# Kernel tuning notes

Measured on AMD Instinct MI355X. Metric: run time of the kernel, lower is better.

The kernel has to match this reference:

```python
import jax, jax.numpy as jnp
import numpy as np

N = 50000      # nodes
E = 800000     # edges per view (before self loops)
F_IN = 256     # node feature dim
H = 4          # attention heads
C = 128        # hidden dim (per-head out_channels; concat=False -> mean over heads)
V = 3          # views
NEG_SLOPE = 0.2


def gat_view(x, edge_index, W, a_src, a_dst, b):
    """PyG-style GATConv(heads=H, concat=False) + ELU. Adds self loops."""
    n = x.shape[0]
    loops = jnp.arange(n, dtype=edge_index.dtype)
    src = jnp.concatenate([edge_index[0], loops])  # [E+N]
    dst = jnp.concatenate([edge_index[1], loops])
    h = (x @ W).reshape(n, H, C)                    # [N,H,C]
    s_src = jnp.sum(h * a_src, axis=-1)             # [N,H]
    s_dst = jnp.sum(h * a_dst, axis=-1)             # [N,H]
    e = jax.nn.leaky_relu(s_src[src] + s_dst[dst], NEG_SLOPE)  # [E+N,H]
    # segment softmax over incoming edges of each destination node
    m = jax.ops.segment_max(e, dst, num_segments=n)
    m = jnp.where(jnp.isfinite(m), m, 0.0)
    ex = jnp.exp(e - m[dst])
    denom = jax.ops.segment_sum(ex, dst, num_segments=n)
    alpha = ex / jnp.maximum(denom[dst], 1e-16)     # [E+N,H]
    out = jax.ops.segment_sum(h[src] * alpha[:, :, None], dst, num_segments=n)  # [N,H,C]
    return jax.nn.elu(out.mean(axis=1) + b)         # [N,C]


def setup_inputs() -> dict:
    key = jax.random.key(0)
    ks = jax.random.split(key, 12)
    d = {
        "x": jax.random.normal(ks[0], (N, F_IN), dtype=jnp.float32),
        "edge_index0": jax.random.randint(ks[1], (2, E), 0, N, dtype=jnp.int32),
        "edge_index1": jax.random.randint(ks[2], (2, E), 0, N, dtype=jnp.int32),
        "edge_index2": jax.random.randint(ks[3], (2, E), 0, N, dtype=jnp.int32),
        "W": jax.random.normal(ks[4], (V, F_IN, H * C), dtype=jnp.float32) * 0.05,
        "a_src": jax.random.normal(ks[5], (V, H, C), dtype=jnp.float32) * 0.05,
        "a_dst": jax.random.normal(ks[6], (V, H, C), dtype=jnp.float32) * 0.05,
        "b": jnp.zeros((V, C), dtype=jnp.float32),
        "fus_w": jax.random.normal(ks[7], (C, 1), dtype=jnp.float32) * 0.05,
        "fus_b": jnp.zeros((1,), dtype=jnp.float32),
        "cls_w1": jax.random.normal(ks[8], (C, C // 2), dtype=jnp.float32) * 0.05,
        "cls_b1": jnp.zeros((C // 2,), dtype=jnp.float32),
        "cls_w2": jax.random.normal(ks[9], (C // 2, 2), dtype=jnp.float32) * 0.05,
        "cls_b2": jnp.zeros((2,), dtype=jnp.float32),
    }
    return d


def reference(x, edge_index0, edge_index1, edge_index2, W, a_src, a_dst, b,
              fus_w, fus_b, cls_w1, cls_b1, cls_w2, cls_b2):
    eis = [edge_index0, edge_index1, edge_index2]
    views = [gat_view(x, eis[v], W[v], a_src[v], a_dst[v], b[v]) for v in range(V)]
    stacked = jnp.stack(views, axis=1)                     # [N,V,C]
    scores = jnp.squeeze(stacked @ fus_w, -1) + fus_b      # [N,V]
    weights = jax.nn.softmax(scores, axis=1)               # view attention
    fused = jnp.sum(stacked * weights[..., None], axis=1)  # [N,C]
    hcls = jax.nn.relu(fused @ cls_w1 + cls_b1)            # dropout = identity (eval)
    logits = hcls @ cls_w2 + cls_b2                        # [N,2]
    return logits, weights
```

## Files before the change

### kernel.cpp

```cpp
#include <hip/hip_runtime.h>
#include <math.h>

#define NN 50000
#define EE 800000
#define FIN 256
#define HH 4
#define CC 128
#define HC 512
#define VV 3

#define NB 196
#define SPB 256
#define CAP 4608
#define EPB 8192

typedef __attribute__((ext_vector_type(8))) short short8;
typedef __attribute__((ext_vector_type(4))) float f32x4;
typedef __attribute__((ext_vector_type(2))) float f32x2;

__device__ __forceinline__ float lrelu(float x){ return x > 0.f ? x : 0.2f*x; }

__device__ __forceinline__ unsigned short f2bf(float f){
  unsigned u = __float_as_uint(f);
  u += 0x7fffu + ((u >> 16) & 1);
  return (unsigned short)(u >> 16);
}
__device__ __forceinline__ float bf2f(short b){
  return __uint_as_float(((unsigned)b & 0xffffu) << 16);
}

__device__ __forceinline__ float wave_sum64(float v){
#pragma unroll
  for (int off = 32; off; off >>= 1) v += __shfl_xor(v, off);
  return v;
}

__device__ __forceinline__ void async16(void* lds, const void* g){
  __builtin_amdgcn_global_load_lds(
      (const __attribute__((address_space(1))) unsigned*)g,
      (__attribute__((address_space(3))) unsigned*)lds, 16, 0, 0);
}

__global__ __launch_bounds__(256) void cast_x(const float* __restrict__ x,
                                              unsigned short* __restrict__ xb){
  int t = blockIdx.x * 256 + threadIdx.x;
  float4 v = *(const float4*)&x[(size_t)t * 4];
  ushort4 o;
  o.x = f2bf(v.x); o.y = f2bf(v.y); o.z = f2bf(v.z); o.w = f2bf(v.w);
  *(ushort4*)&xb[(size_t)t * 4] = o;
}

__global__ __launch_bounds__(256) void prep_w_all(const float* __restrict__ W,
                                                  unsigned short* __restrict__ wp){
  int t = blockIdx.x * 256 + threadIdx.x;
  int v = t >> 17;
  int tl = t & 131071;
  int k = tl >> 9, n = tl & 511;
  wp[(size_t)v * (FIN * HC) + (size_t)(k >> 5) * (HC * 32) + n * 32 + (k & 31)] = f2bf(W[t]);
}

__global__ __launch_bounds__(256) void gemm_mfma_scores(
    const unsigned short* __restrict__ xb, const unsigned short* __restrict__ wp_all,
    unsigned char* __restrict__ hb_all,
    const float* __restrict__ a_src, const float* __restrict__ a_dst,
    float* __restrict__ ssrc_all, float* __restrict__ sdst_all){
  __shared__ short As[128 * 32];
  __shared__ short Bs[128 * 32];
  __shared__ float sred[2][128][2];
  int tid = threadIdx.x;
  int wave = tid >> 6, lane = tid & 63;
  int l16 = lane & 15, q = lane >> 4;
  int wr = wave >> 1, wc = wave & 1;
  int head = blockIdx.y, v = blockIdx.z;
  int rowBase = blockIdx.x * 128, colBase = head * 128;

  const unsigned short* wp = wp_all + (size_t)v * FIN * HC;
  unsigned char* hb = hb_all + (size_t)v * NN * HC;
  const float* a_src_v = a_src + v * HH * CC;
  const float* a_dst_v = a_dst + v * HH * CC;
  float* ssrc = ssrc_all + (size_t)v * NN * HH;
  float* sdst = sdst_all + (size_t)v * NN * HH;

  int off0 = wave * 2048 + lane * 16;
  int off1 = off0 + 1024;
  int arow0 = off0 >> 6, akb0 = (off0 & 63) >> 1;
  int arow1 = off1 >> 6, akb1 = (off1 & 63) >> 1;
  size_t ga0 = (size_t)min(rowBase + arow0, NN - 1) * FIN + akb0;
  size_t ga1 = (size_t)min(rowBase + arow1, NN - 1) * FIN + akb1;
  const unsigned short* wpc = wp + (size_t)colBase * 32;

  f32x4 acc[4][4] = {};
  for (int kt = 0; kt < 8; kt++){
    async16((char*)As + wave * 2048,        xb + ga0 + kt * 32);
    async16((char*)As + wave * 2048 + 1024, xb + ga1 + kt * 32);
    async16((char*)Bs + wave * 2048,        wpc + (size_t)kt * (HC * 32) + (off0 >> 1));
    async16((char*)Bs + wave * 2048 + 1024, wpc + (size_t)kt * (HC * 32) + (off1 >> 1));
    __syncthreads();
    short8 af[4], bf[4];
#pragma unroll
    for (int i = 0; i < 4; i++)
      af[i] = *(const short8*)&As[(wr * 64 + i * 16 + l16) * 32 + q * 8];
#pragma unroll
    for (int j = 0; j < 4; j++)
      bf[j] = *(const short8*)&Bs[(wc * 64 + j * 16 + l16) * 32 + q * 8];
#pragma unroll
    for (int i = 0; i < 4; i++)
#pragma unroll
      for (int j = 0; j < 4; j++)
        acc[i][j] = __builtin_amdgcn_mfma_f32_16x16x32_bf16(af[i], bf[j], acc[i][j], 0, 0, 0);
    __syncthreads();
  }
#pragma unroll
  for (int i = 0; i < 4; i++){
#pragma unroll
    for (int r = 0; r < 4; r++){
      int row = rowBase + wr * 64 + i * 16 + q * 4 + r;
      if (row < NN){
        int p01 = __builtin_amdgcn_cvt_pk_fp8_f32(acc[i][0][r], acc[i][1][r], 0, false);
        int p23 = __builtin_amdgcn_cvt_pk_fp8_f32(acc[i][2][r], acc[i][3][r], 0, false);
        size_t rb = (size_t)row * HC + colBase + wc * 64 + l16;
        hb[rb +  0] = (unsigned char)(p01 & 0xff);
        hb[rb + 16] = (unsigned char)((p01 >> 8) & 0xff);
        hb[rb + 32] = (unsigned char)(p23 & 0xff);
        hb[rb + 48] = (unsigned char)((p23 >> 8) & 0xff);
      }
    }
  }
  float asv[4], adv[4];
#pragma unroll
  for (int j = 0; j < 4; j++){
    int c = wc * 64 + j * 16 + l16;
    asv[j] = a_src_v[head * CC + c];
    adv[j] = a_dst_v[head * CC + c];
  }
  float ps[4][4], pd[4][4];
#pragma unroll
  for (int i = 0; i < 4; i++)
#pragma unroll
    for (int r = 0; r < 4; r++){
      float s = 0.f, d = 0.f;
#pragma unroll
      for (int j = 0; j < 4; j++){
        s = fmaf(acc[i][j][r], asv[j], s);
        d = fmaf(acc[i][j][r], adv[j], d);
      }
      ps[i][r] = s; pd[i][r] = d;
    }
#pragma unroll
  for (int off = 1; off < 16; off <<= 1)
#pragma unroll
    for (int i = 0; i < 4; i++)
#pragma unroll
      for (int r = 0; r < 4; r++){
        ps[i][r] += __shfl_xor(ps[i][r], off);
        pd[i][r] += __shfl_xor(pd[i][r], off);
      }
  if (l16 == 0){
#pragma unroll
    for (int i = 0; i < 4; i++)
#pragma unroll
      for (int r = 0; r < 4; r++){
        int rl = wr * 64 + i * 16 + q * 4 + r;
        sred[wc][rl][0] = ps[i][r];
        sred[wc][rl][1] = pd[i][r];
      }
  }
  __syncthreads();
  if (tid < 128){
    int row = rowBase + tid;
    if (row < NN){
      ssrc[row * HH + head] = sred[0][tid][0] + sred[1][tid][0];
      sdst[row * HH + head] = sred[0][tid][1] + sred[1][tid][1];
    }
  }
}

__global__ __launch_bounds__(256) void bucket_scatter(const int* __restrict__ e0,
    const int* __restrict__ e1, const int* __restrict__ e2,
    int* __restrict__ gcur, unsigned* __restrict__ pairs){
  int v = blockIdx.y;
  const int* ei = (v == 0) ? e0 : ((v == 1) ? e1 : e2);
  __shared__ int cnt[NB];
  __shared__ int base[NB];
  int tid = threadIdx.x;
  for (int i = tid; i < NB; i += 256) cnt[i] = 0;
  __syncthreads();
  int estart = blockIdx.x * EPB;
  int eend = min(estart + EPB, EE);
  for (int e = estart + tid; e < eend; e += 256)
    atomicAdd(&cnt[ei[EE + e] >> 8], 1);
  __syncthreads();
  for (int i = tid; i < NB; i += 256){
    int c = cnt[i];
    base[i] = (c > 0) ? atomicAdd(&gcur[v * NB + i], c) : 0;
    cnt[i] = 0;
  }
  __syncthreads();
  for (int e = estart + tid; e < eend; e += 256){
    int s = ei[e], d = ei[EE + e];
    int b = d >> 8;
    int off = base[b] + atomicAdd(&cnt[b], 1);
    if (off < CAP)
      pairs[(size_t)(v * NB + b) * CAP + off] = ((unsigned)(d & 255) << 16) | (unsigned)s;
  }
}

__global__ __launch_bounds__(256) void bucket_scan(const int* __restrict__ gcur,
                                                   int* __restrict__ bbase){
  int v = blockIdx.x;
  __shared__ int wsum[4];
  int tid = threadIdx.x, lane = tid & 63, wv = tid >> 6;
  int val = 0;
  if (tid < NB) val = min(gcur[v * NB + tid], CAP) + min(SPB, NN - tid * SPB);
  int x = val;
#pragma unroll
  for (int off = 1; off < 64; off <<= 1){
    int t = __shfl_up(x, off);
    if (lane >= off) x += t;
  }
  if (lane == 63) wsum[wv] = x;
  __syncthreads();
  int pre = 0;
#pragma unroll
  for (int w = 0; w < 4; w++) if (w < wv) pre += wsum[w];
  if (tid < NB) bbase[v * NB + tid] = pre + x - val;
}

__global__ __launch_bounds__(256) void bucket_csr(const int* __restrict__ gcur,
    const int* __restrict__ bbase, const unsigned* __restrict__ pairs,
    int* __restrict__ rowptr_all, int* __restrict__ colx_all){
  int v = blockIdx.y, b = blockIdx.x;
  int* rowptr = rowptr_all + v * (NN + 1);
  int* colx = colx_all + (size_t)v * (EE + NN);
  __shared__ int hist[SPB];
  __shared__ int wsum[4];
  __shared__ int lcol[CAP + SPB];
  int tid = threadIdx.x, lane = tid & 63, wv = tid >> 6;
  int node0 = b << 8;
  int nvalid = min(SPB, NN - node0);
  int cnt = min(gcur[v * NB + b], CAP);
  int base = bbase[v * NB + b];
  const unsigned* pp = pairs + (size_t)(v * NB + b) * CAP;
  hist[tid] = (tid < nvalid) ? 1 : 0;
  __syncthreads();
  for (int i = tid; i < cnt; i += 256)
    atomicAdd(&hist[pp[i] >> 16], 1);
  __syncthreads();
  int val = hist[tid];
  int x = val;
#pragma unroll
  for (int off = 1; off < 64; off <<= 1){
    int t = __shfl_up(x, off);
    if (lane >= off) x += t;
  }
  if (lane == 63) wsum[wv] = x;
  __syncthreads();
  int pre = 0;
#pragma unroll
  for (int w = 0; w < 4; w++) if (w < wv) pre += wsum[w];
  int excl = pre + x - val;
  __syncthreads();
  hist[tid] = excl + ((tid < nvalid) ? 1 : 0);
  if (tid < nvalid){
    rowptr[node0 + tid] = base + excl;
    lcol[excl] = node0 + tid;
  }
  __syncthreads();
  for (int i = tid; i < cnt; i += 256){
    unsigned p = pp[i];
    int pos = atomicAdd(&hist[p >> 16], 1);
    lcol[pos] = (int)(p & 0xffffu);
  }
  __syncthreads();
  int total = cnt + nvalid;
  for (int i = tid; i < total; i += 256) colx[base + i] = lcol[i];
  if (b == NB - 1 && tid == 0) rowptr[NN] = base + total;
}

__global__ __launch_bounds__(256) void aggregate(const unsigned char* __restrict__ hb_all,
    const float* __restrict__ ssrc_all, const float* __restrict__ sdst_all,
    const int* __restrict__ rowptr_all, const int* __restrict__ colx_all,
    const float* __restrict__ bb, unsigned short* __restrict__ vout_all){
  int v = blockIdx.y;
  const unsigned char* hb = hb_all + (size_t)v * NN * HC;
  const float* ssrc = ssrc_all + (size_t)v * NN * HH;
  const float* sdst = sdst_all + (size_t)v * NN * HH;
  const int* rowptr = rowptr_all + v * (NN + 1);
  const int* colx = colx_all + (size_t)v * (EE + NN);
  const float* bv = bb + v * CC;
  unsigned short* voutv = vout_all + (size_t)v * NN * CC;

  int wave = threadIdx.x >> 6, lane = threadIdx.x & 63;
  int node = blockIdx.x * 4 + wave;
  int start = rowptr[node];
  int deg = rowptr[node + 1] - start;
  int myh = lane >> 4;
  float sdh = sdst[node * HH + myh];
  float acc[8] = {0.f, 0.f, 0.f, 0.f, 0.f, 0.f, 0.f, 0.f};
  float dsum = 0.f;

#define AGG_FMA(CH, CE) { \
    f32x2 p0 = __builtin_amdgcn_cvt_pk_f32_fp8(CH.x, false); \
    f32x2 p1 = __builtin_amdgcn_cvt_pk_f32_fp8(CH.x, true); \
    f32x2 p2 = __builtin_amdgcn_cvt_pk_f32_fp8(CH.y, false); \
    f32x2 p3 = __builtin_amdgcn_cvt_pk_f32_fp8(CH.y, true); \
    acc[0] = fmaf(CE, p0[0], acc[0]); \
    acc[1] = fmaf(CE, p0[1], acc[1]); \
    acc[2] = fmaf(CE, p1[0], acc[2]); \
    acc[3] = fmaf(CE, p1[1], acc[3]); \
    acc[4] = fmaf(CE, p2[0], acc[4]); \
    acc[5] = fmaf(CE, p2[1], acc[5]); \
    acc[6] = fmaf(CE, p3[0], acc[6]); \
    acc[7] = fmaf(CE, p3[1], acc[7]); }

  if (deg <= 64){
    int cpre = (lane < deg) ? colx[start + lane] : 0;
    uint2 h0, h1, h2, h3, h4, h5, h6, h7;
    float s0, s1, s2, s3, s4, s5, s6, s7;
#define AGG_PRO(HP, SP, P) { \
    int sp = __shfl(cpre, min(P, deg - 1)); \
    HP = *(const uint2*)&hb[(size_t)(unsigned)(sp * HC) + lane * 8]; \
    SP = ssrc[sp * HH + myh]; }
    AGG_PRO(h0, s0, 0) AGG_PRO(h1, s1, 1) AGG_PRO(h2, s2, 2) AGG_PRO(h3, s3, 3)
    AGG_PRO(h4, s4, 4) AGG_PRO(h5, s5, 5) AGG_PRO(h6, s6, 6) AGG_PRO(h7, s7, 7)
#undef AGG_PRO
#define AGG_STEP(HP, SP, P) { \
    float ce = __expf(lrelu(SP + sdh)); \
    dsum += ce; \
    uint2 ch = HP; \
    int ni = i + 8 + P; \
    if (ni < deg){ \
      int ns = __shfl(cpre, ni); \
      HP = *(const uint2*)&hb[(size_t)(unsigned)(ns * HC) + lane * 8]; \
      SP = ssrc[ns * HH + myh]; \
    } \
    AGG_FMA(ch, ce) }
    int i = 0;
    for (; i + 8 <= deg; i += 8){
      AGG_STEP(h0, s0, 0) AGG_STEP(h1, s1, 1) AGG_STEP(h2, s2, 2) AGG_STEP(h3, s3, 3)
      AGG_STEP(h4, s4, 4) AGG_STEP(h5, s5, 5) AGG_STEP(h6, s6, 6) AGG_STEP(h7, s7, 7)
    }
#undef AGG_STEP
    int rem = deg - i;
#define AGG_TAIL(HP, SP, P) if (rem > P){ \
    float ce = __expf(lrelu(SP + sdh)); \
    dsum += ce; \
    AGG_FMA(HP, ce) }
    AGG_TAIL(h0, s0, 0) AGG_TAIL(h1, s1, 1) AGG_TAIL(h2, s2, 2) AGG_TAIL(h3, s3, 3)
    AGG_TAIL(h4, s4, 4) AGG_TAIL(h5, s5, 5) AGG_TAIL(h6, s6, 6)
#undef AGG_TAIL
  } else {
    for (int i = 0; i < deg; i++){
      int src = colx[start + i];
      float sv = ssrc[src * HH + myh];
      float ce = __expf(lrelu(sv + sdh));
      dsum += ce;
      uint2 ch = *(const uint2*)&hb[(size_t)(unsigned)(src * HC) + lane * 8];
      AGG_FMA(ch, ce)
    }
  }
#undef AGG_FMA
  float rinv = 0.25f / fmaxf(dsum, 1e-16f);
#pragma unroll
  for (int j = 0; j < 8; j++) acc[j] *= rinv;
#pragma unroll
  for (int off = 16; off < 64; off <<= 1){
#pragma unroll
    for (int j = 0; j < 8; j++) acc[j] += __shfl_xor(acc[j], off);
  }
  if (lane < 16){
    int c0 = lane * 8;
    short8 o;
#pragma unroll
    for (int j = 0; j < 8; j++){
      float vv = acc[j] + bv[c0 + j];
      float e = vv > 0.f ? vv : (__expf(vv) - 1.f);
      o[j] = (short)f2bf(e);
    }
    *(short8*)&voutv[(size_t)node * CC + c0] = o;
  }
}

__global__ __launch_bounds__(256) void fuse_classify(const unsigned short* __restrict__ vb,
    const float* __restrict__ fw, const float* __restrict__ fb,
    const float* __restrict__ w1, const float* __restrict__ b1,
    const float* __restrict__ w2, const float* __restrict__ b2,
    float* __restrict__ out){
  __shared__ float sw1[CC * 64];
  __shared__ float sfused[4][CC];
  int tid = threadIdx.x;
  for (int i = tid * 4; i < CC * 64; i += 1024)
    *(float4*)&sw1[i] = *(const float4*)&w1[i];
  __syncthreads();
  int wave = tid >> 6, lane = tid & 63;
  int node = blockIdx.x * 4 + wave;
  unsigned r0 = *(const unsigned*)&vb[(size_t)(0 * NN + node) * CC + lane * 2];
  unsigned r1 = *(const unsigned*)&vb[(size_t)(1 * NN + node) * CC + lane * 2];
  unsigned r2 = *(const unsigned*)&vb[(size_t)(2 * NN + node) * CC + lane * 2];
  float v0x = bf2f((short)(r0 & 0xffffu)), v0y = bf2f((short)(r0 >> 16));
  float v1x = bf2f((short)(r1 & 0xffffu)), v1y = bf2f((short)(r1 >> 16));
  float v2x = bf2f((short)(r2 & 0xffffu)), v2y = bf2f((short)(r2 >> 16));
  float fwa = fw[lane * 2], fwb = fw[lane * 2 + 1];
  float s0 = wave_sum64(v0x * fwa + v0y * fwb) + fb[0];
  float s1 = wave_sum64(v1x * fwa + v1y * fwb) + fb[0];
  float s2 = wave_sum64(v2x * fwa + v2y * fwb) + fb[0];
  float mx = fmaxf(s0, fmaxf(s1, s2));
  float e0 = __expf(s0 - mx), e1 = __expf(s1 - mx), e2 = __expf(s2 - mx);
  float rs = 1.f / (e0 + e1 + e2);
  float w0 = e0 * rs, w1v = e1 * rs, w2v = e2 * rs;
  float f0 = w0 * v0x + w1v * v1x + w2v * v2x;
  float f1 = w0 * v0y + w1v * v1y + w2v * v2y;
  sfused[wave][lane * 2]     = f0;
  sfused[wave][lane * 2 + 1] = f1;
  if (lane < 3){
    float wv = (lane == 0) ? w0 : ((lane == 1) ? w1v : w2v);
    out[2 * NN + node * 3 + lane] = wv;
  }
  __syncthreads();
  float hc = b1[lane];
#pragma unroll 8
  for (int c = 0; c < CC; c++)
    hc = fmaf(sfused[wave][c], sw1[c * 64 + lane], hc);
  hc = fmaxf(hc, 0.f);
  float l0 = wave_sum64(hc * w2[lane * 2]);
  float l1 = wave_sum64(hc * w2[lane * 2 + 1]);
  if (lane == 0){
    out[node * 2]     = l0 + b2[0];
    out[node * 2 + 1] = l1 + b2[1];
  }
}

extern "C" void kernel_launch(void* const* d_in, const int* in_sizes, int n_in,
                              void* d_out, int out_size, void* d_ws, size_t ws_size,
                              hipStream_t stream){
  const float* x      = (const float*)d_in[0];
  const int*   e0     = (const int*)d_in[1];
  const int*   e1     = (const int*)d_in[2];
  const int*   e2     = (const int*)d_in[3];
  const float* W      = (const float*)d_in[4];
  const float* a_src  = (const float*)d_in[5];
  const float* a_dst  = (const float*)d_in[6];
  const float* bb     = (const float*)d_in[7];
  const float* fus_w  = (const float*)d_in[8];
  const float* fus_b  = (const float*)d_in[9];
  const float* cls_w1 = (const float*)d_in[10];
  const float* cls_b1 = (const float*)d_in[11];
  const float* cls_w2 = (const float*)d_in[12];
  const float* cls_b2 = (const float*)d_in[13];
  float* out = (float*)d_out;

  unsigned short* xb = (unsigned short*)d_ws;
  unsigned char* hb  = (unsigned char*)(xb + (size_t)NN * FIN);
  unsigned short* wp = (unsigned short*)(hb + (size_t)VV * NN * HC);
  float* ssrc = (float*)(wp + (size_t)VV * FIN * HC);
  float* sdst = ssrc + (size_t)VV * NN * HH;
  int* gcur   = (int*)(sdst + (size_t)VV * NN * HH);
  int* bbase  = gcur + VV * NB;
  int* rowptr = bbase + VV * NB;
  int* colx   = rowptr + VV * (NN + 1);
  unsigned* pairs = (unsigned*)(colx + (size_t)VV * (EE + NN));
  unsigned short* voutb = (unsigned short*)pairs;

  hipMemsetAsync(gcur, 0, (size_t)VV * NB * sizeof(int), stream);
  cast_x<<<12500, 256, 0, stream>>>(x, xb);
  prep_w_all<<<1536, 256, 0, stream>>>(W, wp);
  dim3 p1grid((EE + EPB - 1) / EPB, 3);
  bucket_scatter<<<p1grid, 256, 0, stream>>>(e0, e1, e2, gcur, pairs);
  bucket_scan<<<3, 256, 0, stream>>>(gcur, bbase);
  dim3 p2grid(NB, 3);
  bucket_csr<<<p2grid, 256, 0, stream>>>(gcur, bbase, pairs, rowptr, colx);

  dim3 ggrid(391, 4, 3);
  gemm_mfma_scores<<<ggrid, 256, 0, stream>>>(xb, wp, hb, a_src, a_dst, ssrc, sdst);
  dim3 agrid(12500, 3);
  aggregate<<<agrid, 256, 0, stream>>>(hb, ssrc, sdst, rowptr, colx, bb, voutb);
  fuse_classify<<<12500, 256, 0, stream>>>(voutb, fus_w, fus_b, cls_w1, cls_b1,
                                           cls_w2, cls_b2, out);
}
```

Baseline: 545.4 us.

## Rework GAT aggregation to process two edges per wave with wide fp8 loads

The aggregate kernel now splits each wave into two halves, each handling alternate edges with 16-byte fp8 row loads. It uses packed f32x2 FMAs and exp2 with log2e folded into the attention vectors, and combines the halves with shuffles at the end. Column indices are pre-scaled by 4 so address math is simpler, and the separate high-degree path is merged into one loop that falls back to global index loads. The GEMM drops its LDS staging and syncs in favour of direct register double-buffered global loads. This may cost coalescing or load reuse in the GEMM.

```diff
diff --git a/kernel.cpp b/kernel.cpp
--- a/kernel.cpp
+++ b/kernel.cpp
@@ -8,6 +8,7 @@
 #define CC 128
 #define HC 512
 #define VV 3
+#define LOG2E 1.4426950408889634f
 
 #define NB 196
 #define SPB 256
@@ -18,8 +19,6 @@
 typedef __attribute__((ext_vector_type(4))) float f32x4;
 typedef __attribute__((ext_vector_type(2))) float f32x2;
 
-__device__ __forceinline__ float lrelu(float x){ return x > 0.f ? x : 0.2f*x; }
-
 __device__ __forceinline__ unsigned short f2bf(float f){
   unsigned u = __float_as_uint(f);
   u += 0x7fffu + ((u >> 16) & 1);
@@ -33,12 +32,6 @@
 #pragma unroll
   for (int off = 32; off; off >>= 1) v += __shfl_xor(v, off);
   return v;
-}
-
-__device__ __forceinline__ void async16(void* lds, const void* g){
-  __builtin_amdgcn_global_load_lds(
-      (const __attribute__((address_space(1))) unsigned*)g,
-      (__attribute__((address_space(3))) unsigned*)lds, 16, 0, 0);
 }
 
 __global__ __launch_bounds__(256) void cast_x(const float* __restrict__ x,
@@ -64,8 +57,6 @@
     unsigned char* __restrict__ hb_all,
     const float* __restrict__ a_src, const float* __restrict__ a_dst,
     float* __restrict__ ssrc_all, float* __restrict__ sdst_all){
-  __shared__ short As[128 * 32];
-  __shared__ short Bs[128 * 32];
   __shared__ float sred[2][128][2];
   int tid = threadIdx.x;
   int wave = tid >> 6, lane = tid & 63;
@@ -81,34 +72,40 @@
   float* ssrc = ssrc_all + (size_t)v * NN * HH;
   float* sdst = sdst_all + (size_t)v * NN * HH;
 
-  int off0 = wave * 2048 + lane * 16;
-  int off1 = off0 + 1024;
-  int arow0 = off0 >> 6, akb0 = (off0 & 63) >> 1;
-  int arow1 = off1 >> 6, akb1 = (off1 & 63) >> 1;
-  size_t ga0 = (size_t)min(rowBase + arow0, NN - 1) * FIN + akb0;
-  size_t ga1 = (size_t)min(rowBase + arow1, NN - 1) * FIN + akb1;
-  const unsigned short* wpc = wp + (size_t)colBase * 32;
-
+  const unsigned short* ap[4];
+  const unsigned short* bp[4];
+#pragma unroll
+  for (int i = 0; i < 4; i++){
+    int row = min(rowBase + wr * 64 + i * 16 + l16, NN - 1);
+    ap[i] = xb + (size_t)row * FIN + q * 8;
+  }
+#pragma unroll
+  for (int j = 0; j < 4; j++){
+    int col = colBase + wc * 64 + j * 16 + l16;
+    bp[j] = wp + (size_t)col * 32 + q * 8;
+  }
+  short8 af[2][4], bf[2][4];
+#pragma unroll
+  for (int i = 0; i < 4; i++){
+    af[0][i] = *(const short8*)(ap[i]);
+    bf[0][i] = *(const short8*)(bp[i]);
+  }
   f32x4 acc[4][4] = {};
+#pragma unroll
   for (int kt = 0; kt < 8; kt++){
-    async16((char*)As + wave * 2048,        xb + ga0 + kt * 32);
-    async16((char*)As + wave * 2048 + 1024, xb + ga1 + kt * 32);
-    async16((char*)Bs + wave * 2048,        wpc + (size_t)kt * (HC * 32) + (off0 >> 1));
-    async16((char*)Bs + wave * 2048 + 1024, wpc + (size_t)kt * (HC * 32) + (off1 >> 1));
-    __syncthreads();
-    short8 af[4], bf[4];
+    int cur = kt & 1, nxt = cur ^ 1;
+    if (kt < 7){
+#pragma unroll
+      for (int i = 0; i < 4; i++){
+        af[nxt][i] = *(const short8*)(ap[i] + (kt + 1) * 32);
+        bf[nxt][i] = *(const short8*)(bp[i] + (size_t)(kt + 1) * (HC * 32));
+      }
+    }
 #pragma unroll
     for (int i = 0; i < 4; i++)
-      af[i] = *(const short8*)&As[(wr * 64 + i * 16 + l16) * 32 + q * 8];
-#pragma unroll
-    for (int j = 0; j < 4; j++)
-      bf[j] = *(const short8*)&Bs[(wc * 64 + j * 16 + l16) * 32 + q * 8];
-#pragma unroll
-    for (int i = 0; i < 4; i++)
 #pragma unroll
       for (int j = 0; j < 4; j++)
-        acc[i][j] = __builtin_amdgcn_mfma_f32_16x16x32_bf16(af[i], bf[j], acc[i][j], 0, 0, 0);
-    __syncthreads();
+        acc[i][j] = __builtin_amdgcn_mfma_f32_16x16x32_bf16(af[cur][i], bf[cur][j], acc[i][j], 0, 0, 0);
   }
 #pragma unroll
   for (int i = 0; i < 4; i++){
@@ -130,8 +127,8 @@
 #pragma unroll
   for (int j = 0; j < 4; j++){
     int c = wc * 64 + j * 16 + l16;
-    asv[j] = a_src_v[head * CC + c];
-    adv[j] = a_dst_v[head * CC + c];
+    asv[j] = a_src_v[head * CC + c] * LOG2E;
+    adv[j] = a_dst_v[head * CC + c] * LOG2E;
   }
   float ps[4][4], pd[4][4];
 #pragma unroll
@@ -263,13 +260,13 @@
   hist[tid] = excl + ((tid < nvalid) ? 1 : 0);
   if (tid < nvalid){
     rowptr[node0 + tid] = base + excl;
-    lcol[excl] = node0 + tid;
+    lcol[excl] = (node0 + tid) << 2;
   }
   __syncthreads();
   for (int i = tid; i < cnt; i += 256){
     unsigned p = pp[i];
     int pos = atomicAdd(&hist[p >> 16], 1);
-    lcol[pos] = (int)(p & 0xffffu);
+    lcol[pos] = (int)(p & 0xffffu) << 2;
   }
   __syncthreads();
   int total = cnt + nvalid;
@@ -287,97 +284,97 @@
   const float* sdst = sdst_all + (size_t)v * NN * HH;
   const int* rowptr = rowptr_all + v * (NN + 1);
   const int* colx = colx_all + (size_t)v * (EE + NN);
-  const float* bv = bb + v * CC;
-  unsigned short* voutv = vout_all + (size_t)v * NN * CC;
 
   int wave = threadIdx.x >> 6, lane = threadIdx.x & 63;
   int node = blockIdx.x * 4 + wave;
   int start = rowptr[node];
   int deg = rowptr[node + 1] - start;
-  int myh = lane >> 4;
-  float sdh = sdst[node * HH + myh];
-  float acc[8] = {0.f, 0.f, 0.f, 0.f, 0.f, 0.f, 0.f, 0.f};
+  int half = lane >> 5;
+  int cl = lane & 31;
+  int hsel = cl >> 3;
+  int cl16 = cl * 16;
+  float sdh = sdst[node * HH + hsel];
+  f32x2 acc2[8] = {};
   float dsum = 0.f;
-
-#define AGG_FMA(CH, CE) { \
-    f32x2 p0 = __builtin_amdgcn_cvt_pk_f32_fp8(CH.x, false); \
-    f32x2 p1 = __builtin_amdgcn_cvt_pk_f32_fp8(CH.x, true); \
-    f32x2 p2 = __builtin_amdgcn_cvt_pk_f32_fp8(CH.y, false); \
-    f32x2 p3 = __builtin_amdgcn_cvt_pk_f32_fp8(CH.y, true); \
-    acc[0] = fmaf(CE, p0[0], acc[0]); \
-    acc[1] = fmaf(CE, p0[1], acc[1]); \
-    acc[2] = fmaf(CE, p1[0], acc[2]); \
-    acc[3] = fmaf(CE, p1[1], acc[3]); \
-    acc[4] = fmaf(CE, p2[0], acc[4]); \
-    acc[5] = fmaf(CE, p2[1], acc[5]); \
-    acc[6] = fmaf(CE, p3[0], acc[6]); \
-    acc[7] = fmaf(CE, p3[1], acc[7]); }
-
-  if (deg <= 64){
-    int cpre = (lane < deg) ? colx[start + lane] : 0;
-    uint2 h0, h1, h2, h3, h4, h5, h6, h7;
-    float s0, s1, s2, s3, s4, s5, s6, s7;
-#define AGG_PRO(HP, SP, P) { \
-    int sp = __shfl(cpre, min(P, deg - 1)); \
-    HP = *(const uint2*)&hb[(size_t)(unsigned)(sp * HC) + lane * 8]; \
-    SP = ssrc[sp * HH + myh]; }
-    AGG_PRO(h0, s0, 0) AGG_PRO(h1, s1, 1) AGG_PRO(h2, s2, 2) AGG_PRO(h3, s3, 3)
-    AGG_PRO(h4, s4, 4) AGG_PRO(h5, s5, 5) AGG_PRO(h6, s6, 6) AGG_PRO(h7, s7, 7)
-#undef AGG_PRO
-#define AGG_STEP(HP, SP, P) { \
-    float ce = __expf(lrelu(SP + sdh)); \
-    dsum += ce; \
-    uint2 ch = HP; \
-    int ni = i + 8 + P; \
+  int cpre = (lane < deg) ? colx[start + lane] : 0;
+  int S = (deg + 1) >> 1;
+  uint4 hv[4]; float sv[4];
+#pragma unroll
+  for (int p = 0; p < 4; p++){
+    int si = min(2 * p + half, deg - 1);
+    int sp4 = __shfl(cpre, si);
+    hv[p] = *(const uint4*)&hb[((size_t)(unsigned)sp4 << 7) + cl16];
+    sv[p] = ssrc[sp4 + hsel];
+  }
+#define AGG_CVT_FMA(CH, E2) { \
+    acc2[0] = __builtin_elementwise_fma(E2, __builtin_amdgcn_cvt_pk_f32_fp8(CH.x, false), acc2[0]); \
+    acc2[1] = __builtin_elementwise_fma(E2, __builtin_amdgcn_cvt_pk_f32_fp8(CH.x, true),  acc2[1]); \
+    acc2[2] = __builtin_elementwise_fma(E2, __builtin_amdgcn_cvt_pk_f32_fp8(CH.y, false), acc2[2]); \
+    acc2[3] = __builtin_elementwise_fma(E2, __builtin_amdgcn_cvt_pk_f32_fp8(CH.y, true),  acc2[3]); \
+    acc2[4] = __builtin_elementwise_fma(E2, __builtin_amdgcn_cvt_pk_f32_fp8(CH.z, false), acc2[4]); \
+    acc2[5] = __builtin_elementwise_fma(E2, __builtin_amdgcn_cvt_pk_f32_fp8(CH.z, true),  acc2[5]); \
+    acc2[6] = __builtin_elementwise_fma(E2, __builtin_amdgcn_cvt_pk_f32_fp8(CH.w, false), acc2[6]); \
+    acc2[7] = __builtin_elementwise_fma(E2, __builtin_amdgcn_cvt_pk_f32_fp8(CH.w, true),  acc2[7]); }
+#define AGG_STEP(P) { \
+    int si = 2 * (i + P) + half; \
+    float xx = sv[P] + sdh; \
+    float e = __builtin_amdgcn_exp2f(fmaxf(xx, 0.2f * xx)); \
+    e = (si < deg) ? e : 0.f; \
+    dsum += e; \
+    uint4 ch = hv[P]; \
+    int ni = 2 * (i + P + 4) + half; \
     if (ni < deg){ \
-      int ns = __shfl(cpre, ni); \
-      HP = *(const uint2*)&hb[(size_t)(unsigned)(ns * HC) + lane * 8]; \
-      SP = ssrc[ns * HH + myh]; \
+      int sp4; \
+      if (ni < 64) sp4 = __shfl(cpre, ni); else sp4 = colx[start + ni]; \
+      hv[P] = *(const uint4*)&hb[((size_t)(unsigned)sp4 << 7) + cl16]; \
+      sv[P] = ssrc[sp4 + hsel]; \
     } \
-    AGG_FMA(ch, ce) }
-    int i = 0;
-    for (; i + 8 <= deg; i += 8){
-      AGG_STEP(h0, s0, 0) AGG_STEP(h1, s1, 1) AGG_STEP(h2, s2, 2) AGG_STEP(h3, s3, 3)
-      AGG_STEP(h4, s4, 4) AGG_STEP(h5, s5, 5) AGG_STEP(h6, s6, 6) AGG_STEP(h7, s7, 7)
+    f32x2 e2 = {e, e}; \
+    AGG_CVT_FMA(ch, e2) }
+#define AGG_TAIL(P) { \
+    int si = 2 * (i + P) + half; \
+    float xx = sv[P] + sdh; \
+    float e = __builtin_amdgcn_exp2f(fmaxf(xx, 0.2f * xx)); \
+    e = (si < deg) ? e : 0.f; \
+    dsum += e; \
+    uint4 ch = hv[P]; \
+    f32x2 e2 = {e, e}; \
+    AGG_CVT_FMA(ch, e2) }
+  int i = 0;
+  for (; i + 4 <= S; i += 4){
+    AGG_STEP(0) AGG_STEP(1) AGG_STEP(2) AGG_STEP(3)
+  }
+  int rem = S - i;
+  if (rem > 0) AGG_TAIL(0)
+  if (rem > 1) AGG_TAIL(1)
+  if (rem > 2) AGG_TAIL(2)
+#undef AGG_STEP
+#undef AGG_TAIL
+#undef AGG_CVT_FMA
+  dsum += __shfl_xor(dsum, 32);
+  float rinv = 0.25f / fmaxf(dsum, 1e-16f);
+#pragma unroll
+  for (int j = 0; j < 8; j++){
+    float o0 = acc2[j][0] * rinv, o1 = acc2[j][1] * rinv;
+    o0 += __shfl_xor(o0, 32); o1 += __shfl_xor(o1, 32);
+    o0 += __shfl_xor(o0, 8);  o1 += __shfl_xor(o1, 8);
+    o0 += __shfl_xor(o0, 16); o1 += __shfl_xor(o1, 16);
+    acc2[j][0] = o0; acc2[j][1] = o1;
+  }
+  if (lane < 8){
+    const float* bv = bb + v * CC;
+    unsigned short* voutv = vout_all + (size_t)v * NN * CC;
+    unsigned ow[8];
+#pragma unroll
+    for (int j = 0; j < 8; j++){
+      float v0 = acc2[j][0] + bv[cl16 + 2 * j];
+      float v1 = acc2[j][1] + bv[cl16 + 2 * j + 1];
+      v0 = v0 > 0.f ? v0 : (__expf(v0) - 1.f);
+      v1 = v1 > 0.f ? v1 : (__expf(v1) - 1.f);
+      ow[j] = (unsigned)f2bf(v0) | ((unsigned)f2bf(v1) << 16);
     }
-#undef AGG_STEP
-    int rem = deg - i;
-#define AGG_TAIL(HP, SP, P) if (rem > P){ \
-    float ce = __expf(lrelu(SP + sdh)); \
-    dsum += ce; \
-    AGG_FMA(HP, ce) }
-    AGG_TAIL(h0, s0, 0) AGG_TAIL(h1, s1, 1) AGG_TAIL(h2, s2, 2) AGG_TAIL(h3, s3, 3)
-    AGG_TAIL(h4, s4, 4) AGG_TAIL(h5, s5, 5) AGG_TAIL(h6, s6, 6)
-#undef AGG_TAIL
-  } else {
-    for (int i = 0; i < deg; i++){
-      int src = colx[start + i];
-      float sv = ssrc[src * HH + myh];
-      float ce = __expf(lrelu(sv + sdh));
-      dsum += ce;
-      uint2 ch = *(const uint2*)&hb[(size_t)(unsigned)(src * HC) + lane * 8];
-      AGG_FMA(ch, ce)
-    }
-  }
-#undef AGG_FMA
-  float rinv = 0.25f / fmaxf(dsum, 1e-16f);
-#pragma unroll
-  for (int j = 0; j < 8; j++) acc[j] *= rinv;
-#pragma unroll
-  for (int off = 16; off < 64; off <<= 1){
-#pragma unroll
-    for (int j = 0; j < 8; j++) acc[j] += __shfl_xor(acc[j], off);
-  }
-  if (lane < 16){
-    int c0 = lane * 8;
-    short8 o;
-#pragma unroll
-    for (int j = 0; j < 8; j++){
-      float vv = acc[j] + bv[c0 + j];
-      float e = vv > 0.f ? vv : (__expf(vv) - 1.f);
-      o[j] = (short)f2bf(e);
-    }
-    *(short8*)&voutv[(size_t)node * CC + c0] = o;
+    *(uint4*)&voutv[(size_t)node * CC + cl16]     = make_uint4(ow[0], ow[1], ow[2], ow[3]);
+    *(uint4*)&voutv[(size_t)node * CC + cl16 + 8] = make_uint4(ow[4], ow[5], ow[6], ow[7]);
   }
 }
 
```

Measured after the change: 639.4 us. 1.17x slower.
